# Optimization experiments

Hardware: AMD Instinct MI355X
Metric: run time of the kernel (lower is better)

The kernel has to match this reference:

```python
import jax, jax.numpy as jnp
import numpy as np

B, L, C, D, H = 32, 4096, 64, 512, 720
EPS = 1e-5

def _xavier(key, shape):
    fan_in, fan_out = shape
    lim = float(np.sqrt(6.0 / (fan_in + fan_out)))
    return jax.random.uniform(key, shape, minval=-lim, maxval=lim, dtype=jnp.float32)

def setup_inputs() -> dict:
    key = jax.random.key(0)
    ks = jax.random.split(key, 8)
    return {
        "x": jax.random.normal(ks[0], (B, L, C), dtype=jnp.float32),
        "alpha": jnp.full((C,), 0.5, dtype=jnp.float32),
        "rev_w": jnp.ones((C,), dtype=jnp.float32),
        "rev_b": jnp.zeros((C,), dtype=jnp.float32),
        "se_w": _xavier(ks[1], (C, D)), "se_b": jnp.zeros((D,), jnp.float32),
        "sp_w": _xavier(ks[2], (D, C)), "sp_b": jnp.zeros((C,), jnp.float32),
        "st_w": _xavier(ks[3], (L, H)), "st_b": jnp.zeros((H,), jnp.float32),
        "te_w": _xavier(ks[4], (C, D)), "te_b": jnp.zeros((D,), jnp.float32),
        "tp_w": _xavier(ks[5], (D, C)), "tp_b": jnp.zeros((C,), jnp.float32),
        "tt_w": _xavier(ks[6], (L, H)), "tt_b": jnp.zeros((H,), jnp.float32),
    }

def _path(z, ew, eb, pw, pb, tw, tb):
    # z: (B,L,C) -> embed C->D -> (identity backbone) -> proj D->C -> temporal L->H
    h = z @ ew + eb            # (B,L,D)
    h = h @ pw + pb            # (B,L,C)
    h = jnp.einsum('blc,lh->bhc', h, tw) + tb[None, :, None]  # (B,H,C)
    return h

def reference(x, alpha, rev_w, rev_b, se_w, se_b, sp_w, sp_b, st_w, st_b,
              te_w, te_b, tp_w, tp_b, tt_w, tt_b):
    # RevIN norm (stats detached, var unbiased=False)
    mean = jax.lax.stop_gradient(jnp.mean(x, axis=1, keepdims=True))          # (B,1,C)
    stdev = jax.lax.stop_gradient(jnp.sqrt(jnp.var(x, axis=1, keepdims=True) + EPS))
    xn = (x - mean) / stdev * rev_w + rev_b
    # EMA decomposition: trend[t] = a*trend[t-1] + (1-a)*x[t], trend[0]=x[0]
    a = jax.nn.sigmoid(alpha)  # (C,)
    def step(carry, xt):
        nxt = a * carry + (1.0 - a) * xt
        return nxt, nxt
    t0 = xn[:, 0]                                    # (B,C)
    _, tr = jax.lax.scan(step, t0, jnp.swapaxes(xn, 0, 1)[1:])  # (L-1,B,C)
    trend = jnp.swapaxes(jnp.concatenate([t0[None], tr], axis=0), 0, 1)  # (B,L,C)
    seasonal = xn - trend
    out = _path(seasonal, se_w, se_b, sp_w, sp_b, st_w, st_b) \
        + _path(trend,    te_w, te_b, tp_w, tp_b, tt_w, tt_b)   # (B,H,C)
    # RevIN denorm
    out = (out - rev_b) / (rev_w + EPS)
    out = out * stdev + mean
    return out
```

## Files before the change

kernel.cpp:

```cpp
#include <hip/hip_runtime.h>
#include <hip/hip_bf16.h>
#include <string.h>
#include <stdint.h>

typedef __hip_bfloat16 bf16_t;
typedef float f32x4 __attribute__((ext_vector_type(4)));
typedef short bf16x8 __attribute__((ext_vector_type(8)));

#define AS_GLOBAL __attribute__((address_space(1)))
#define AS_LDS    __attribute__((address_space(3)))

static constexpr int Bn = 32, Ln = 4096, Cn = 64, Hn = 720, HPn = 768;
static constexpr float EPSf = 1e-5f;

static constexpr size_t OSR_SLICE = (size_t)Bn * Hn * Cn;

__device__ __forceinline__ short f2bf(float f) {
  bf16_t h = __float2bfloat16(f);
  unsigned short u; memcpy(&u, &h, 2);
  return (short)u;
}

__device__ __forceinline__ float sigm(float v) { return 1.f / (1.f + expf(-v)); }

__global__ void __launch_bounds__(256) k_prep(const float* __restrict__ se_w, const float* __restrict__ sp_w,
                                              const float* __restrict__ se_b, const float* __restrict__ sp_b,
                                              const float* __restrict__ te_w, const float* __restrict__ tp_w,
                                              const float* __restrict__ te_b, const float* __restrict__ tp_b,
                                              float* __restrict__ M, float* __restrict__ cvec) {
  int p = blockIdx.y, dc = blockIdx.x, t = threadIdx.x;
  const float* ew = p ? te_w : se_w;
  const float* pw = p ? tp_w : sp_w;
  const float* eb = p ? te_b : se_b;
  const float* pb = p ? tp_b : sp_b;
  int d0 = dc * 64;
  __shared__ float ews[64][68];
  __shared__ float pws[64][68];
  __shared__ float ebs[64];
#pragma unroll
  for (int q = 0; q < 4; ++q) {
    int fi = t * 4 + q;
    int r = fi >> 4, dd = (fi * 4) & 63;
    *reinterpret_cast<f32x4*>(&ews[r][dd]) = *reinterpret_cast<const f32x4*>(&ew[r * 512 + d0 + dd]);
    int pdd = fi >> 4, c = (fi * 4) & 63;
    *reinterpret_cast<f32x4*>(&pws[pdd][c]) = *reinterpret_cast<const f32x4*>(&pw[(d0 + pdd) * 64 + c]);
  }
  if (t < 64) ebs[t] = eb[d0 + t];
  __syncthreads();
  int r0 = (t >> 4) * 4, c0 = (t & 15) * 4;
  float acc[4][4];
#pragma unroll
  for (int i = 0; i < 4; ++i)
#pragma unroll
    for (int j = 0; j < 4; ++j) acc[i][j] = 0.f;
#pragma unroll 4
  for (int g = 0; g < 16; ++g) {
    int dd = g * 4;
    f32x4 av[4], bv[4];
#pragma unroll
    for (int i = 0; i < 4; ++i) av[i] = *reinterpret_cast<const f32x4*>(&ews[r0 + i][dd]);
#pragma unroll
    for (int d = 0; d < 4; ++d) bv[d] = *reinterpret_cast<const f32x4*>(&pws[dd + d][c0]);
#pragma unroll
    for (int d = 0; d < 4; ++d)
#pragma unroll
      for (int i = 0; i < 4; ++i)
#pragma unroll
        for (int j = 0; j < 4; ++j) acc[i][j] = fmaf(av[i][d], bv[d][j], acc[i][j]);
  }
#pragma unroll
  for (int i = 0; i < 4; ++i)
#pragma unroll
    for (int j = 0; j < 4; ++j)
      atomicAdd(&M[p * 4096 + (r0 + i) * 64 + c0 + j], acc[i][j]);
  if (t < 64) {
    float s = (dc == 0) ? pb[t] : 0.f;
#pragma unroll 8
    for (int dd = 0; dd < 64; ++dd) s = fmaf(ebs[dd], pws[dd][t], s);
    atomicAdd(&cvec[p * 64 + t], s);
  }
}

__global__ void k_wprep(const float* __restrict__ st_w, const float* __restrict__ tt_w,
                        bf16_t* __restrict__ Wt, float* __restrict__ S) {
  int p = blockIdx.z;
  const float* W = p ? tt_w : st_w;
  int l0 = blockIdx.x * 64, h0 = blockIdx.y * 64;
  __shared__ float tile[64][65];
  int row = threadIdx.x >> 6, col = threadIdx.x & 63;
  int h = h0 + col;
  float partial = 0.f;
  for (int r = row; r < 64; r += 4) {
    float v = (h < Hn) ? W[(size_t)(l0 + r) * Hn + h] : 0.f;
    tile[r][col] = v;
    partial += v;
  }
  if (h < Hn) atomicAdd(&S[p * 768 + h], partial);
  __syncthreads();
  short* AF = (short*)Wt + (size_t)p * HPn * Ln;
#pragma unroll
  for (int u = 0; u < 2; ++u) {
    int uid = u * 256 + threadIdx.x;
    int ln = uid & 63, ktl = (uid >> 6) & 1, htl = uid >> 7;
    int fr = ln & 15, hi = ln >> 4;
    int ll = ktl * 32 + hi * 8;
    int hh = htl * 16 + fr;
    bf16x8 v;
#pragma unroll
    for (int e = 0; e < 8; ++e) v[e] = f2bf(tile[ll + e][hh]);
    size_t ht = (size_t)(h0 >> 4) + htl, ktg = (size_t)(l0 >> 5) + ktl;
    *reinterpret_cast<bf16x8*>(&AF[((ht * 128 + ktg) << 9) + ((size_t)ln << 3)]) = v;
  }
}

__global__ void __launch_bounds__(256) k_scanA(const float* __restrict__ x, const float* __restrict__ alpha,
                                               float* __restrict__ Psub, float* __restrict__ Pseg,
                                               float* __restrict__ Ssum, float* __restrict__ Ssq) {
  int b = blockIdx.x, q = threadIdx.y, s = blockIdx.y * 4 + q, t = threadIdx.x;
  int c4 = (t & 15) * 4, sub = t >> 4;
  float a[4], k1[4];
#pragma unroll
  for (int i = 0; i < 4; ++i) { a[i] = sigm(alpha[c4 + i]); k1[i] = 1.f - a[i]; }
  const float* xb = x + ((size_t)b * Ln + s * 64 + sub * 16) * Cn + c4;
  float pr[4] = {0.f, 0.f, 0.f, 0.f}, sm[4] = {0.f, 0.f, 0.f, 0.f}, sq[4] = {0.f, 0.f, 0.f, 0.f};
#pragma unroll
  for (int j = 0; j < 16; ++j) {
    f32x4 v = *reinterpret_cast<const f32x4*>(xb + (size_t)j * Cn);
#pragma unroll
    for (int i = 0; i < 4; ++i) {
      sm[i] += v[i];
      sq[i] = fmaf(v[i], v[i], sq[i]);
      pr[i] = fmaf(a[i], pr[i], k1[i] * v[i]);
    }
  }
  *reinterpret_cast<f32x4*>(&Psub[(((size_t)b * 64 + s) * 4 + sub) * 64 + c4]) =
      (f32x4){pr[0], pr[1], pr[2], pr[3]};
  __shared__ float lp[4][4][64], ls[4][4][64], lq[4][4][64];
#pragma unroll
  for (int i = 0; i < 4; ++i) { lp[q][sub][c4 + i] = pr[i]; ls[q][sub][c4 + i] = sm[i]; lq[q][sub][c4 + i] = sq[i]; }
  __syncthreads();
  int c = t;
  float av = sigm(alpha[c]);
  float a16 = av * av; a16 *= a16; a16 *= a16; a16 *= a16;
  float P = ((lp[q][0][c] * a16 + lp[q][1][c]) * a16 + lp[q][2][c]) * a16 + lp[q][3][c];
  int idx = (b * 64 + s) * 64 + c;
  Pseg[idx] = P;
  Ssum[idx] = ls[q][0][c] + ls[q][1][c] + ls[q][2][c] + ls[q][3][c];
  Ssq[idx]  = lq[q][0][c] + lq[q][1][c] + lq[q][2][c] + lq[q][3][c];
}

__global__ void __launch_bounds__(64) k_scanB(const float* __restrict__ x, const float* __restrict__ alpha,
                                              const float* __restrict__ rev_w, const float* __restrict__ rev_b,
                                              const float* __restrict__ Pseg, const float* __restrict__ Ssum,
                                              const float* __restrict__ Ssq,
                                              float* __restrict__ mean, float* __restrict__ rstd,
                                              float* __restrict__ stdv, float* __restrict__ CarryIn) {
  int b = blockIdx.x, c = threadIdx.x;
  float sm = 0.f, sq = 0.f;
#pragma unroll 8
  for (int s = 0; s < 64; ++s) {
    int idx = (b * 64 + s) * 64 + c;
    sm += Ssum[idx]; sq += Ssq[idx];
  }
  float mn = sm * (1.f / 4096.f);
  float var = sq * (1.f / 4096.f) - mn * mn;
  float sd = sqrtf(var + EPSf);
  float rs = 1.f / sd;
  mean[b * 64 + c] = mn; stdv[b * 64 + c] = sd; rstd[b * 64 + c] = rs;

  float w = rev_w[c], rb = rev_b[c];
  float g = rs * w, d = rb - mn * g;
  float a = sigm(alpha[c]);
  float a2 = a * a, a4 = a2 * a2, a8 = a4 * a4, a16 = a8 * a8, a32 = a16 * a16;
  float a64 = a32 * a32;
  float dk1s = d * (1.f - a64);
  float carry = fmaf(g, x[((size_t)b * Ln) * Cn + c], d);
  for (int so = 0; so < 8; ++so) {
    float pv[8];
#pragma unroll
    for (int i = 0; i < 8; ++i)
      pv[i] = Pseg[((size_t)(b * 64 + so * 8 + i)) * 64 + c];
#pragma unroll
    for (int i = 0; i < 8; ++i) {
      CarryIn[((size_t)(b * 64 + so * 8 + i)) * 64 + c] = carry;
      carry = fmaf(a64, carry, fmaf(g, pv[i], dk1s));
    }
  }
}

__global__ void __launch_bounds__(256) k_scanC(const float* __restrict__ x, const float* __restrict__ alpha,
                                               const float* __restrict__ rev_w, const float* __restrict__ rev_b,
                                               const float* __restrict__ mean, const float* __restrict__ rstd,
                                               const float* __restrict__ CarryIn, const float* __restrict__ Psub,
                                               bf16_t* __restrict__ Zt) {
  int b = blockIdx.x, s = blockIdx.y * 4 + threadIdx.y, t = threadIdx.x;
  int c4 = (t & 15) * 4, sub = t >> 4;
  float g[4], d[4], a[4], k1[4], a16[4], dk[4], tr[4];
#pragma unroll
  for (int i = 0; i < 4; ++i) {
    int c = c4 + i;
    float rs = rstd[b * 64 + c];
    g[i] = rs * rev_w[c]; d[i] = rev_b[c] - mean[b * 64 + c] * g[i];
    a[i] = sigm(alpha[c]); k1[i] = 1.f - a[i];
    float v = a[i] * a[i]; v *= v; v *= v; v *= v;
    a16[i] = v;
    dk[i] = d[i] * (1.f - v);
  }
  f32x4 cs = *reinterpret_cast<const f32x4*>(&CarryIn[((size_t)b * 64 + s) * 64 + c4]);
#pragma unroll
  for (int i = 0; i < 4; ++i) tr[i] = cs[i];
  for (int k = 0; k < sub; ++k) {
    f32x4 p = *reinterpret_cast<const f32x4*>(&Psub[(((size_t)b * 64 + s) * 4 + k) * 64 + c4]);
#pragma unroll
    for (int i = 0; i < 4; ++i) tr[i] = fmaf(a16[i], tr[i], fmaf(g[i], p[i], dk[i]));
  }
  const float* xb = x + ((size_t)b * Ln + s * 64 + sub * 16) * Cn + c4;
  bf16x8 vs[4][2], vt[4][2];
#pragma unroll
  for (int j = 0; j < 16; ++j) {
    f32x4 v = *reinterpret_cast<const f32x4*>(xb + (size_t)j * Cn);
#pragma unroll
    for (int i = 0; i < 4; ++i) {
      float xn = fmaf(g[i], v[i], d[i]);
      tr[i] = fmaf(a[i], tr[i], k1[i] * xn);
      vs[i][j >> 3][j & 7] = f2bf(xn - tr[i]);
      vt[i][j >> 3][j & 7] = f2bf(tr[i]);
    }
  }
#pragma unroll
  for (int i = 0; i < 4; ++i) {
    int c = c4 + i;
    bf16_t* zs = Zt + ((size_t)b * 64 + c) * Ln + s * 64 + sub * 16;
    bf16_t* zt = zs + (size_t)Bn * Cn * Ln;
    *reinterpret_cast<bf16x8*>(zs) = vs[i][0];
    *reinterpret_cast<bf16x8*>(zs + 8) = vs[i][1];
    *reinterpret_cast<bf16x8*>(zt) = vt[i][0];
    *reinterpret_cast<bf16x8*>(zt + 8) = vt[i][1];
  }
}

__device__ __forceinline__ void gload16(const bf16_t* g, bf16_t* l) {
  __builtin_amdgcn_global_load_lds((const AS_GLOBAL uint32_t*)g, (AS_LDS uint32_t*)l, 16, 0, 0);
}

template <int KS>
__global__ void __launch_bounds__(256, 3) k_gemm(const bf16_t* __restrict__ Wt, const bf16_t* __restrict__ Zt,
                                                 float* __restrict__ Osr) {
  int per = gridDim.x >> 3;
  int swz = (blockIdx.x & 7) * per + (blockIdx.x >> 3);
  int z = swz / 96, rem = swz % 96;
  int by = rem >> 4, bx = rem & 15;
  int p = z / KS, kq = z % KS;
  const short* AF = (const short*)Wt + (size_t)p * HPn * Ln;
  const bf16_t* Bz = Zt + (size_t)p * (Bn * Cn) * Ln;
  int h0 = by * 128, n0 = bx * 128;
  int kbase = kq * (Ln / KS);
  const int NT = (Ln / KS) / 32;
  __shared__ __align__(16) bf16_t Bl[3][128 * 32];
  int tid = threadIdx.x, wid = tid >> 6, lane = tid & 63;
  int wr = wid >> 1, wc = wid & 1;
  int fr = lane & 15, hi = lane >> 4;
  int kc = (tid & 3) ^ ((tid >> 3) & 3);
  const bf16_t* bbase = Bz + (size_t)(n0 + (tid >> 2)) * Ln + kbase + kc * 8;
  const short* abase = AF + ((((size_t)(h0 >> 4) + wr * 4) * 128 + (kbase >> 5)) << 9) + ((size_t)lane << 3);

  f32x4 acc[4][4];
#pragma unroll
  for (int i = 0; i < 4; ++i)
#pragma unroll
    for (int j = 0; j < 4; ++j) acc[i][j] = (f32x4){0.f, 0.f, 0.f, 0.f};

  auto STAGE_B = [&](int bufi, int kt) {
    gload16(bbase + (size_t)kt * 32, &Bl[bufi][tid * 8]);
    gload16(bbase + (size_t)64 * Ln + kt * 32, &Bl[bufi][2048 + tid * 8]);
  };
  auto ALOAD = [&](bf16x8 (&dst)[4], int kt) {
#pragma unroll
    for (int i = 0; i < 4; ++i)
      dst[i] = *reinterpret_cast<const bf16x8*>(abase + (((size_t)i * 128 + kt) << 9));
  };

  int sw8 = (hi ^ ((fr >> 1) & 3)) * 8;
  auto COMPUTE = [&](int bufi, const bf16x8 (&af)[4]) {
    bf16x8 bfr[4];
#pragma unroll
    for (int j = 0; j < 4; ++j)
      bfr[j] = *reinterpret_cast<const bf16x8*>(&Bl[bufi][(wc * 64 + j * 16 + fr) * 32 + sw8]);
    __builtin_amdgcn_s_setprio(1);
#pragma unroll
    for (int i = 0; i < 4; ++i)
#pragma unroll
      for (int j = 0; j < 4; ++j)
        acc[i][j] = __builtin_amdgcn_mfma_f32_16x16x32_bf16(af[i], bfr[j], acc[i][j], 0, 0, 0);
    __builtin_amdgcn_s_setprio(0);
  };

  bf16x8 aA[4], aB[4];
  STAGE_B(0, 0);
  STAGE_B(1, 1);
  ALOAD(aA, 0);

  auto ITER = [&](int t, int cur, int nx, const bf16x8 (&acur)[4], bf16x8 (&anxt)[4]) {
    __builtin_amdgcn_sched_barrier(0);
    if (t + 1 < NT) { asm volatile("s_waitcnt vmcnt(6)" ::: "memory"); }
    else            { asm volatile("s_waitcnt vmcnt(4)" ::: "memory"); }
    __builtin_amdgcn_s_barrier();
    __builtin_amdgcn_sched_barrier(0);
    if (t + 2 < NT) STAGE_B(nx, t + 2);
    if (t + 1 < NT) ALOAD(anxt, t + 1);
    COMPUTE(cur, acur);
  };

  int cur = 0;
  for (int t = 0; t < NT; t += 2) {
    int c1 = (cur == 2) ? 0 : cur + 1;
    int nx0 = (c1 == 2) ? 0 : c1 + 1;
    int nx1 = cur;
    ITER(t,     cur, nx0, aA, aB);
    ITER(t + 1, c1,  nx1, aB, aA);
    cur = nx0;
  }

#pragma unroll
  for (int i = 0; i < 4; ++i) {
#pragma unroll
    for (int j = 0; j < 4; ++j) {
#pragma unroll
      for (int r = 0; r < 4; ++r) {
        int m = wr * 64 + i * 16 + hi * 4 + r;
        int h = h0 + m;
        if (h < Hn) {
          int n = n0 + wc * 64 + j * 16 + fr;
          int bidx = n >> 6, c = n & 63;
          Osr[(((size_t)z * Bn + bidx) * Hn + h) * Cn + c] = acc[i][j][r];
        }
      }
    }
  }
}

template <int KS>
__global__ void __launch_bounds__(256) k_epi(const float* __restrict__ Osr, const float* __restrict__ M,
                                             const float* __restrict__ cvec, const float* __restrict__ S,
                                             const float* __restrict__ st_b, const float* __restrict__ tt_b,
                                             const float* __restrict__ rev_w, const float* __restrict__ rev_b,
                                             const float* __restrict__ mean, const float* __restrict__ stdv,
                                             float* __restrict__ out) {
  __shared__ float Msh[2][64][64];
  __shared__ float rowS[32][64];
  __shared__ float rowT[32][64];
  int t = threadIdx.x;
  for (int i = t; i < 8192; i += 256) ((float*)Msh)[i] = M[i];
  int c = t & 63, grp = t >> 6;
  float w = rev_w[c], rb = rev_b[c];
  float cs = cvec[c], ct = cvec[64 + c];
  int base = blockIdx.x * 32;
#pragma unroll
  for (int k = 0; k < 8; ++k) {
    int rl = grp * 8 + k;
    int r = base + rl;
    int b = r / 720, h = r % 720;
    float vs = 0.f, vt = 0.f;
#pragma unroll
    for (int kq = 0; kq < KS; ++kq) {
      vs += Osr[(((size_t)kq * Bn + b) * Hn + h) * Cn + c];
      vt += Osr[(((size_t)(KS + kq) * Bn + b) * Hn + h) * Cn + c];
    }
    rowS[rl][c] = vs;
    rowT[rl][c] = vt;
  }
  __syncthreads();
  float acc[8];
  int hh[8], bb[8];
#pragma unroll
  for (int k = 0; k < 8; ++k) {
    int r = base + grp * 8 + k;
    bb[k] = r / 720; hh[k] = r % 720;
    acc[k] = cs * S[hh[k]] + ct * S[768 + hh[k]] + st_b[hh[k]] + tt_b[hh[k]];
  }
  int r0 = grp * 8;
#pragma unroll 4
  for (int cp = 0; cp < 64; ++cp) {
    float m0 = Msh[0][cp][c], m1 = Msh[1][cp][c];
#pragma unroll
    for (int k = 0; k < 8; ++k)
      acc[k] = fmaf(rowS[r0 + k][cp], m0, fmaf(rowT[r0 + k][cp], m1, acc[k]));
  }
  float winv = 1.f / (w + EPSf);
#pragma unroll
  for (int k = 0; k < 8; ++k) {
    float o = (acc[k] - rb) * winv * stdv[bb[k] * Cn + c] + mean[bb[k] * Cn + c];
    out[(size_t)(base + r0 + k) * 64 + c] = o;
  }
}

extern "C" void kernel_launch(void* const* d_in, const int* in_sizes, int n_in,
                              void* d_out, int out_size, void* d_ws, size_t ws_size,
                              hipStream_t stream) {
  const float* x     = (const float*)d_in[0];
  const float* alpha = (const float*)d_in[1];
  const float* rev_w = (const float*)d_in[2];
  const float* rev_b = (const float*)d_in[3];
  const float* se_w  = (const float*)d_in[4];
  const float* se_b  = (const float*)d_in[5];
  const float* sp_w  = (const float*)d_in[6];
  const float* sp_b  = (const float*)d_in[7];
  const float* st_w  = (const float*)d_in[8];
  const float* st_b  = (const float*)d_in[9];
  const float* te_w  = (const float*)d_in[10];
  const float* te_b  = (const float*)d_in[11];
  const float* tp_w  = (const float*)d_in[12];
  const float* tp_b  = (const float*)d_in[13];
  const float* tt_w  = (const float*)d_in[14];
  const float* tt_b  = (const float*)d_in[15];
  float* out = (float*)d_out;

  const size_t SZ_WT  = (size_t)2 * HPn * Ln * 2;
  const size_t SZ_ZT  = (size_t)2 * Bn * Cn * Ln * 2;
  const size_t SZ_SEG = (size_t)Bn * 64 * 64 * 4;
  const size_t SZ_M   = 2 * 64 * 64 * 4;
  const size_t SZ_CV  = 2 * 64 * 4;
  const size_t SZ_S   = 2 * 768 * 4;
  const size_t TAIL   = SZ_M + SZ_CV + SZ_S + 3 * (size_t)Bn * Cn * 4;

  const size_t NEED4 = SZ_WT + SZ_ZT + 8 * OSR_SLICE * 4 + TAIL;
  const int KS = (ws_size >= NEED4) ? 4 : 1;
  const size_t SZ_OSR = (size_t)(2 * KS) * OSR_SLICE * 4;

  char* ws = (char*)d_ws;
  bf16_t* Wt   = (bf16_t*)(ws);
  bf16_t* Zt   = (bf16_t*)(ws + SZ_WT);
  float*  Osr  = (float*)(ws + SZ_WT + SZ_ZT);
  float*  Psub  = Osr;
  float*  Pseg  = (float*)((char*)Psub + 4 * SZ_SEG);
  float*  Ssum  = (float*)((char*)Pseg + SZ_SEG);
  float*  Ssq   = (float*)((char*)Ssum + SZ_SEG);
  float*  Carry = (float*)((char*)Ssq + SZ_SEG);
  char* tail = ws + SZ_WT + SZ_ZT + SZ_OSR;
  float* Mbuf = (float*)tail;                 tail += SZ_M;
  float* cvec = (float*)tail;                 tail += SZ_CV;
  float* S    = (float*)tail;                 tail += SZ_S;
  float* mean = (float*)tail;                 tail += (size_t)Bn * Cn * 4;
  float* rstd = (float*)tail;                 tail += (size_t)Bn * Cn * 4;
  float* stdv = (float*)tail;

  hipMemsetAsync(Mbuf, 0, SZ_M + SZ_CV + SZ_S, stream);

  k_prep<<<dim3(8, 2), 256, 0, stream>>>(se_w, sp_w, se_b, sp_b, te_w, tp_w, te_b, tp_b, Mbuf, cvec);
  k_wprep<<<dim3(64, 12, 2), 256, 0, stream>>>(st_w, tt_w, Wt, S);
  k_scanA<<<dim3(32, 16), dim3(64, 4), 0, stream>>>(x, alpha, Psub, Pseg, Ssum, Ssq);
  k_scanB<<<32, 64, 0, stream>>>(x, alpha, rev_w, rev_b, Pseg, Ssum, Ssq, mean, rstd, stdv, Carry);
  k_scanC<<<dim3(32, 16), dim3(64, 4), 0, stream>>>(x, alpha, rev_w, rev_b, mean, rstd, Carry, Psub, Zt);
  if (KS == 4) {
    k_gemm<4><<<768, 256, 0, stream>>>(Wt, Zt, Osr);
    k_epi<4><<<720, 256, 0, stream>>>(Osr, Mbuf, cvec, S, st_b, tt_b, rev_w, rev_b, mean, stdv, out);
  } else {
    k_gemm<1><<<192, 256, 0, stream>>>(Wt, Zt, Osr);
    k_epi<1><<<720, 256, 0, stream>>>(Osr, Mbuf, cvec, S, st_b, tt_b, rev_w, rev_b, mean, stdv, out);
  }
}
```

Baseline: 108.1 us.

## Store Z operand in MFMA fragment layout and load B directly to registers

The decomposition kernel now writes the seasonal/trend bf16 operand in the same pre-swizzled fragment layout already used for the weights, so each lane can load its MFMA B fragment with a single 16-byte global load. The GEMM drops the LDS triple buffer, the global_load_lds staging, the waitcnt/barrier pipeline and the LDS fragment reads, and uses a simple register double-buffered loop instead. This removes LDS traffic and block-wide barriers. The cost is that B data is no longer shared across waves through LDS, so each wave fetches its own B fragments from global/L2, and latency hiding now relies only on register prefetch one step ahead.

Measured after the change: 114.4 us. 5.8% more time.

```diff
diff --git a/kernel.cpp b/kernel.cpp
--- a/kernel.cpp
+++ b/kernel.cpp
@@ -6,9 +6,6 @@
 typedef __hip_bfloat16 bf16_t;
 typedef float f32x4 __attribute__((ext_vector_type(4)));
 typedef short bf16x8 __attribute__((ext_vector_type(8)));
-
-#define AS_GLOBAL __attribute__((address_space(1)))
-#define AS_LDS    __attribute__((address_space(3)))
 
 static constexpr int Bn = 32, Ln = 4096, Cn = 64, Hn = 720, HPn = 768;
 static constexpr float EPSf = 1e-5f;
@@ -227,20 +224,22 @@
       vt[i][j >> 3][j & 7] = f2bf(tr[i]);
     }
   }
+  short* BF0 = (short*)Zt;
+  const size_t PATH = (size_t)Bn * Cn * Ln;
+  int nt = b * 4 + (c4 >> 4);
+  int ktg = s * 2 + (sub >> 1);
+  int hb = (sub & 1) * 2;
+  size_t u0 = (((size_t)nt * 128 + ktg) << 9);
 #pragma unroll
   for (int i = 0; i < 4; ++i) {
-    int c = c4 + i;
-    bf16_t* zs = Zt + ((size_t)b * 64 + c) * Ln + s * 64 + sub * 16;
-    bf16_t* zt = zs + (size_t)Bn * Cn * Ln;
-    *reinterpret_cast<bf16x8*>(zs) = vs[i][0];
-    *reinterpret_cast<bf16x8*>(zs + 8) = vs[i][1];
-    *reinterpret_cast<bf16x8*>(zt) = vt[i][0];
-    *reinterpret_cast<bf16x8*>(zt + 8) = vt[i][1];
-  }
-}
-
-__device__ __forceinline__ void gload16(const bf16_t* g, bf16_t* l) {
-  __builtin_amdgcn_global_load_lds((const AS_GLOBAL uint32_t*)g, (AS_LDS uint32_t*)l, 16, 0, 0);
+    int frv = (c4 & 15) + i;
+    size_t o0 = u0 + (((size_t)(hb * 16 + frv)) << 3);
+    size_t o1 = u0 + (((size_t)((hb + 1) * 16 + frv)) << 3);
+    *reinterpret_cast<bf16x8*>(BF0 + o0) = vs[i][0];
+    *reinterpret_cast<bf16x8*>(BF0 + o1) = vs[i][1];
+    *reinterpret_cast<bf16x8*>(BF0 + PATH + o0) = vt[i][0];
+    *reinterpret_cast<bf16x8*>(BF0 + PATH + o1) = vt[i][1];
+  }
 }
 
 template <int KS>
@@ -252,17 +251,15 @@
   int by = rem >> 4, bx = rem & 15;
   int p = z / KS, kq = z % KS;
   const short* AF = (const short*)Wt + (size_t)p * HPn * Ln;
-  const bf16_t* Bz = Zt + (size_t)p * (Bn * Cn) * Ln;
+  const short* BF = (const short*)Zt + (size_t)p * (Bn * Cn) * Ln;
   int h0 = by * 128, n0 = bx * 128;
   int kbase = kq * (Ln / KS);
   const int NT = (Ln / KS) / 32;
-  __shared__ __align__(16) bf16_t Bl[3][128 * 32];
   int tid = threadIdx.x, wid = tid >> 6, lane = tid & 63;
   int wr = wid >> 1, wc = wid & 1;
   int fr = lane & 15, hi = lane >> 4;
-  int kc = (tid & 3) ^ ((tid >> 3) & 3);
-  const bf16_t* bbase = Bz + (size_t)(n0 + (tid >> 2)) * Ln + kbase + kc * 8;
-  const short* abase = AF + ((((size_t)(h0 >> 4) + wr * 4) * 128 + (kbase >> 5)) << 9) + ((size_t)lane << 3);
+  const short* ab = AF + ((((size_t)(h0 >> 4) + wr * 4) * 128 + (kbase >> 5)) << 9) + ((size_t)lane << 3);
+  const short* bb = BF + ((((size_t)(n0 >> 4) + wc * 4) * 128 + (kbase >> 5)) << 9) + ((size_t)lane << 3);
 
   f32x4 acc[4][4];
 #pragma unroll
@@ -270,55 +267,31 @@
 #pragma unroll
     for (int j = 0; j < 4; ++j) acc[i][j] = (f32x4){0.f, 0.f, 0.f, 0.f};
 
-  auto STAGE_B = [&](int bufi, int kt) {
-    gload16(bbase + (size_t)kt * 32, &Bl[bufi][tid * 8]);
-    gload16(bbase + (size_t)64 * Ln + kt * 32, &Bl[bufi][2048 + tid * 8]);
+  auto LOAD = [&](bf16x8 (&a)[4], bf16x8 (&b)[4], int kt) {
+#pragma unroll
+    for (int i = 0; i < 4; ++i)
+      a[i] = *reinterpret_cast<const bf16x8*>(ab + (((size_t)i * 128 + kt) << 9));
+#pragma unroll
+    for (int j = 0; j < 4; ++j)
+      b[j] = *reinterpret_cast<const bf16x8*>(bb + (((size_t)j * 128 + kt) << 9));
   };
-  auto ALOAD = [&](bf16x8 (&dst)[4], int kt) {
+  auto COMPUTE = [&](const bf16x8 (&a)[4], const bf16x8 (&b)[4]) {
+    __builtin_amdgcn_s_setprio(1);
 #pragma unroll
     for (int i = 0; i < 4; ++i)
-      dst[i] = *reinterpret_cast<const bf16x8*>(abase + (((size_t)i * 128 + kt) << 9));
-  };
-
-  int sw8 = (hi ^ ((fr >> 1) & 3)) * 8;
-  auto COMPUTE = [&](int bufi, const bf16x8 (&af)[4]) {
-    bf16x8 bfr[4];
-#pragma unroll
-    for (int j = 0; j < 4; ++j)
-      bfr[j] = *reinterpret_cast<const bf16x8*>(&Bl[bufi][(wc * 64 + j * 16 + fr) * 32 + sw8]);
-    __builtin_amdgcn_s_setprio(1);
-#pragma unroll
-    for (int i = 0; i < 4; ++i)
 #pragma unroll
       for (int j = 0; j < 4; ++j)
-        acc[i][j] = __builtin_amdgcn_mfma_f32_16x16x32_bf16(af[i], bfr[j], acc[i][j], 0, 0, 0);
+        acc[i][j] = __builtin_amdgcn_mfma_f32_16x16x32_bf16(a[i], b[j], acc[i][j], 0, 0, 0);
     __builtin_amdgcn_s_setprio(0);
   };
 
-  bf16x8 aA[4], aB[4];
-  STAGE_B(0, 0);
-  STAGE_B(1, 1);
-  ALOAD(aA, 0);
-
-  auto ITER = [&](int t, int cur, int nx, const bf16x8 (&acur)[4], bf16x8 (&anxt)[4]) {
-    __builtin_amdgcn_sched_barrier(0);
-    if (t + 1 < NT) { asm volatile("s_waitcnt vmcnt(6)" ::: "memory"); }
-    else            { asm volatile("s_waitcnt vmcnt(4)" ::: "memory"); }
-    __builtin_amdgcn_s_barrier();
-    __builtin_amdgcn_sched_barrier(0);
-    if (t + 2 < NT) STAGE_B(nx, t + 2);
-    if (t + 1 < NT) ALOAD(anxt, t + 1);
-    COMPUTE(cur, acur);
-  };
-
-  int cur = 0;
+  bf16x8 aA[4], bA[4], aB[4], bB[4];
+  LOAD(aA, bA, 0);
   for (int t = 0; t < NT; t += 2) {
-    int c1 = (cur == 2) ? 0 : cur + 1;
-    int nx0 = (c1 == 2) ? 0 : c1 + 1;
-    int nx1 = cur;
-    ITER(t,     cur, nx0, aA, aB);
-    ITER(t + 1, c1,  nx1, aB, aA);
-    cur = nx0;
+    if (t + 1 < NT) LOAD(aB, bB, t + 1);
+    COMPUTE(aA, bA);
+    if (t + 2 < NT) LOAD(aA, bA, t + 2);
+    if (t + 1 < NT) COMPUTE(aB, bB);
   }
 
 #pragma unroll
```
